# Kernel optimization log

Measured on AMD Instinct MI355X. Metric: run time of the kernel, lower is better.

Reference implementation:

```python
import jax, jax.numpy as jnp
import numpy as np

D = 256; HD = 16; G = 16; L = 2; HOP = 2; HK = 4
N = 16384; E = 49152; B = 256
VA = 128; VB = 8
SQRT2PI = float(np.sqrt(2.0 * 3.14159))  # module uses pi=3.14159


def group_norm(x, g=G, eps=1e-5):
    # torch GroupNorm(affine=False) on [N, D, 1]: normalize over each group of D//g channels
    n, d = x.shape
    xg = x.reshape(n, g, d // g)
    m = xg.mean(-1, keepdims=True)
    v = ((xg - m) ** 2).mean(-1, keepdims=True)
    return ((xg - m) * jax.lax.rsqrt(v + eps)).reshape(n, d)


def glin(x, w):
    # grouped 1x1 conv (no bias): x [n, g*din], w [g, dout, din] -> [n, g*dout]
    g, dout, din = w.shape
    return jnp.einsum('ngd,god->ngo', x.reshape(-1, g, din), w).reshape(-1, g * dout)


def multi_embed(idx, tables):
    # OGB-style encoder: sum of per-feature embeddings. idx [M,F], tables [F,V,D]
    out = tables[0][idx[:, 0]]
    for f in range(1, tables.shape[0]):
        out = out + tables[f][idx[:, f]]
    return out


def glb(x, pre_w, pre_b, gate_w, val_w, post_w, post_b):
    # GatedLinearBlock (dropout is identity in eval)
    xx = group_norm(x @ pre_w.T + pre_b)
    xx = jax.nn.relu(glin(xx, gate_w)) * glin(xx, val_w)
    return xx @ post_w.T + post_b


def glb2(xg, xv, gate_w, val_w, post_w, post_b):
    # GatedLinearBlock2: separate gate/value inputs, GroupNorm first
    gg = jax.nn.relu(glin(group_norm(xg), gate_w))
    vv = glin(group_norm(xv), val_w)
    return (gg * vv) @ post_w.T + post_b


def forward_impl(x_feat, edge_index, edge_attr, batch, batch_size,
                 edge_distance, atom_emb, bond2d_emb, gauss_means, gauss_stds,
                 attn_w, attn_b, scale_both,
                 conv_bond_emb, conv_pre_w, conv_gate_w, conv_val_w, conv_post_w, conv_post_b, conv_scale,
                 virt_pre_w, virt_pre_b, virt_gate_w, virt_val_w, virt_post_w, virt_post_b, virt_scale,
                 att_pre_w, att_pre_b, att_q_w, att_k_w, att_v_w, att_post_w, att_post_b, att_scale,
                 main_pre_w, main_pre_b, main_gate_w, main_val_w, main_post_w, main_post_b):
    src, dst = edge_index[0], edge_index[1]
    n = x_feat.shape[0]
    deg = jnp.clip(jax.ops.segment_sum(jnp.ones_like(dst), dst, num_segments=n) - 1, 0, 3)
    # --- edge features, mode='both': fuse 2D bond embedding with 3D gaussian features ---
    h2d = multi_embed(edge_attr, bond2d_emb)                      # [E, D]
    std = jnp.abs(gauss_stds) + 0.01
    diff = (edge_distance[:, None] - gauss_means[None, :]) / std
    h3d = jnp.exp(-0.5 * diff * diff) / (SQRT2PI * std)          # [E, D]
    w = jax.nn.sigmoid(jnp.concatenate([h2d, h3d], axis=-1) @ attn_w + attn_b[0])[:, None]
    h_e = w * h2d + (1.0 - w) * h3d
    h_in = jnp.exp(scale_both)[deg] * jax.ops.segment_sum(h_e, dst, num_segments=n)
    h_in = multi_embed(x_feat, atom_emb) + h_in                   # [N, D]
    h_virt = jnp.zeros((batch_size, D), h_in.dtype)
    h_att = jnp.zeros((batch_size, 2 * D // HD, HD, HD), h_in.dtype)
    for l in range(L):
        # --- ConvMessage: hop*kernel gated message-passing sublayers ---
        x_raw, x_out = h_in, jnp.zeros_like(h_in)
        for k in range(HK):
            if k > 0 and k % HOP == 0:
                x_raw, x_out = h_in + x_out, jnp.zeros_like(h_in)
            bond = multi_embed(edge_attr, conv_bond_emb[l, k])
            xp = x_raw @ conv_pre_w[l, k].T
            msg = glb2(xp[dst] + bond, xp[src] + bond,
                       conv_gate_w[l, k], conv_val_w[l, k], conv_post_w[l, k], conv_post_b[l, k])
            x_raw = jax.ops.segment_sum(msg, dst, num_segments=n)
            x_out = x_out + jnp.exp(conv_scale[l, k])[deg] * x_raw
        h_out = h_in + x_out
        # --- VirtMessage: graph-level virtual node with residual state ---
        h_virt = jax.ops.segment_sum(h_in, batch, num_segments=batch_size) + h_virt
        h_out = h_out + (jnp.exp(virt_scale[l]) * glb(h_virt, virt_pre_w[l], virt_pre_b[l],
                          virt_gate_w[l], virt_val_w[l], virt_post_w[l], virt_post_b[l]))[batch]
        # --- AttMessage: linear attention with per-graph scatter normalization ---
        xv0 = group_norm(h_in @ att_pre_w[l].T + att_pre_b[l])
        xq = jnp.exp(glin(xv0, att_q_w[l]) / np.sqrt(HD)).reshape(n, -1, HD)   # [N,32,16]
        xk = jnp.exp(glin(xv0, att_k_w[l]) / np.sqrt(HD)).reshape(n, -1, HD)
        xv = glin(xv0, att_v_w[l]).reshape(n, -1, HD)
        xkv = jnp.einsum('bnh,bnv->bnhv', xk, xv)                               # [N,32,16,16]
        h_att = jax.ops.segment_sum(xkv, batch, num_segments=batch_size) + h_att
        xk_sum = jax.ops.segment_sum(xk, batch, num_segments=batch_size)[batch]
        xq = xq / jnp.einsum('bnh,bnh->bn', xq, xk_sum)[:, :, None]
        att_out = jnp.einsum('bnh,bnhv->bnv', xq, h_att[batch]).reshape(n, 2 * D)
        h_out = h_out + jnp.exp(att_scale[l]) * (att_out @ att_post_w[l].T + att_post_b[l])
        # --- main gated block ---
        h_in = glb(h_out, main_pre_w[l], main_pre_b[l],
                   main_gate_w[l], main_val_w[l], main_post_w[l], main_post_b[l])
    return h_in


def setup_inputs() -> dict:
    key = jax.random.key(0)
    ks = iter(jax.random.split(key, 80))
    def rn(shape, s=0.05):
        return jax.random.normal(next(ks), shape, dtype=jnp.float32) * s
    inp = {}
    inp['x_feat'] = jax.random.randint(next(ks), (N, 9), 0, VA)
    inp['edge_index'] = jax.random.randint(next(ks), (2, E), 0, N)
    inp['edge_attr'] = jax.random.randint(next(ks), (E, 3), 0, VB)
    inp['batch'] = jnp.sort(jax.random.randint(next(ks), (N,), 0, B))
    inp['batch_size'] = B
    inp['edge_distance'] = jax.random.uniform(next(ks), (E,), dtype=jnp.float32) * 4.0
    inp['atom_emb'] = rn((9, VA, D))
    inp['bond2d_emb'] = rn((3, VB, D))
    inp['gauss_means'] = jax.random.uniform(next(ks), (D,), minval=2.0, maxval=3.0)
    inp['gauss_stds'] = jax.random.uniform(next(ks), (D,), minval=1.0, maxval=1.5)
    inp['attn_w'] = rn((2 * D,))
    inp['attn_b'] = rn((1,))
    inp['scale_both'] = jnp.full((4, D), np.log(0.1), jnp.float32)
    inp['conv_bond_emb'] = rn((L, HK, 3, VB, D))
    inp['conv_pre_w'] = rn((L, HK, D, D))
    inp['conv_gate_w'] = rn((L, HK, G, HD, HD))
    inp['conv_val_w'] = rn((L, HK, G, HD, HD))
    inp['conv_post_w'] = rn((L, HK, D, D))
    inp['conv_post_b'] = rn((L, HK, D))
    inp['conv_scale'] = jnp.full((L, HK, 4, D), np.log(0.1), jnp.float32)
    inp['virt_pre_w'] = rn((L, D, D)); inp['virt_pre_b'] = rn((L, D))
    inp['virt_gate_w'] = rn((L, G, 2 * HD, HD)); inp['virt_val_w'] = rn((L, G, 2 * HD, HD))
    inp['virt_post_w'] = rn((L, D, 2 * D)); inp['virt_post_b'] = rn((L, D))
    inp['virt_scale'] = jnp.full((L, D), np.log(0.01), jnp.float32)
    inp['att_pre_w'] = rn((L, D, D)); inp['att_pre_b'] = rn((L, D))
    inp['att_q_w'] = rn((L, G, 2 * HD, HD)); inp['att_k_w'] = rn((L, G, 2 * HD, HD)); inp['att_v_w'] = rn((L, G, 2 * HD, HD))
    inp['att_post_w'] = rn((L, D, 2 * D)); inp['att_post_b'] = rn((L, D))
    inp['att_scale'] = jnp.full((L, D), np.log(0.01), jnp.float32)
    inp['main_pre_w'] = rn((L, D, D)); inp['main_pre_b'] = rn((L, D))
    inp['main_gate_w'] = rn((L, G, 3 * HD, HD)); inp['main_val_w'] = rn((L, G, 3 * HD, HD))
    inp['main_post_w'] = rn((L, D, 3 * D)); inp['main_post_b'] = rn((L, D))
    return inp


def reference(x_feat, edge_index, edge_attr, batch, batch_size, edge_distance,
              atom_emb, bond2d_emb, gauss_means, gauss_stds, attn_w, attn_b, scale_both,
              conv_bond_emb, conv_pre_w, conv_gate_w, conv_val_w, conv_post_w, conv_post_b, conv_scale,
              virt_pre_w, virt_pre_b, virt_gate_w, virt_val_w, virt_post_w, virt_post_b, virt_scale,
              att_pre_w, att_pre_b, att_q_w, att_k_w, att_v_w, att_post_w, att_post_b, att_scale,
              main_pre_w, main_pre_b, main_gate_w, main_val_w, main_post_w, main_post_b):
    return forward_impl(x_feat, edge_index, edge_attr, batch, batch_size,
                        edge_distance, atom_emb, bond2d_emb, gauss_means, gauss_stds,
                        attn_w, attn_b, scale_both,
                        conv_bond_emb, conv_pre_w, conv_gate_w, conv_val_w, conv_post_w, conv_post_b, conv_scale,
                        virt_pre_w, virt_pre_b, virt_gate_w, virt_val_w, virt_post_w, virt_post_b, virt_scale,
                        att_pre_w, att_pre_b, att_q_w, att_k_w, att_v_w, att_post_w, att_post_b, att_scale,
                        main_pre_w, main_pre_b, main_gate_w, main_val_w, main_post_w, main_post_b)
```

## Files before the change

### kernel.cpp

```cpp
#include <hip/hip_runtime.h>
#include <cstdint>
#include <cstddef>
#include <type_traits>

#define NN 16384
#define EE 49152
#define BB 256

typedef _Float16 f16;
typedef _Float16 half8 __attribute__((ext_vector_type(8)));
typedef _Float16 half4v __attribute__((ext_vector_type(4)));
typedef _Float16 half2v __attribute__((ext_vector_type(2)));
typedef float floatx4 __attribute__((ext_vector_type(4)));

#if defined(__has_builtin)
#if __has_builtin(__builtin_amdgcn_fdot2)
#define HAVE_FDOT2 1
#endif
#endif

static constexpr size_t ND = (size_t)NN * 256;


__global__ __launch_bounds__(256) void count_deg_kernel(const int* __restrict__ dst, int* __restrict__ cnt, int e) {
  int i = blockIdx.x * 256 + threadIdx.x;
  if (i < e) atomicAdd(&cnt[dst[i]], 1);
}
__global__ __launch_bounds__(256) void clip_deg_kernel(const int* __restrict__ cnt, int* __restrict__ deg, int n) {
  int i = blockIdx.x * 256 + threadIdx.x;
  if (i < n) { int v = cnt[i] - 1; deg[i] = v < 0 ? 0 : (v > 3 ? 3 : v); }
}
__global__ __launch_bounds__(256) void goff_kernel(const int* __restrict__ batch, int* __restrict__ goff, int n, int b) {
  int i = blockIdx.x * 256 + threadIdx.x;
  if (i > n) return;
  int cur = (i < n) ? batch[i] : b;
  int prev = (i == 0) ? -1 : batch[i - 1];
  for (int x = prev + 1; x <= cur; x++) goff[x] = i;
}
__global__ __launch_bounds__(256) void scan_off_kernel(const int* __restrict__ cnt, int* __restrict__ off) {
  __shared__ int part[256];
  int tid = threadIdx.x;
  int base = tid * 64;
  int s = 0;
  for (int i = 0; i < 64; i++) s += cnt[base + i];
  part[tid] = s;
  __syncthreads();
  for (int o = 1; o < 256; o <<= 1) {
    int t = (tid >= o) ? part[tid - o] : 0;
    __syncthreads();
    part[tid] += t;
    __syncthreads();
  }
  int run = (tid == 0) ? 0 : part[tid - 1];
  for (int i = 0; i < 64; i++) {
    off[base + i] = run;
    run += cnt[base + i];
  }
  if (tid == 255) off[NN] = run;
}
__global__ __launch_bounds__(256) void copy_i_kernel(const int* __restrict__ a, int* __restrict__ b, int n) {
  int i = blockIdx.x * 256 + threadIdx.x;
  if (i < n) b[i] = a[i];
}
__global__ __launch_bounds__(256) void fill_elist_kernel(const int* __restrict__ dst,
    int* __restrict__ cursor, int* __restrict__ elist, int e) {
  int i = blockIdx.x * 256 + threadIdx.x;
  if (i < e) {
    int p = atomicAdd(&cursor[dst[i]], 1);
    elist[p] = i;
  }
}
__global__ __launch_bounds__(256) void gather_edges_kernel(const int* __restrict__ elist,
    const int* __restrict__ eattr, const int* __restrict__ src, const int* __restrict__ dst,
    const float* __restrict__ edist, int* __restrict__ ea_s, int* __restrict__ src_s,
    int* __restrict__ dst_s, float* __restrict__ ed_s) {
  int j = blockIdx.x * 256 + threadIdx.x;
  if (j >= EE) return;
  int e = elist[j];
  ea_s[j * 3 + 0] = eattr[e * 3 + 0];
  ea_s[j * 3 + 1] = eattr[e * 3 + 1];
  ea_s[j * 3 + 2] = eattr[e * 3 + 2];
  src_s[j] = src[e];
  dst_s[j] = dst[e];
  ed_s[j] = edist[e];
}
__global__ __launch_bounds__(256) void add3h_kernel(f16* __restrict__ dstH,
    const float* __restrict__ a, const float* __restrict__ b, int n4) {
  int i = blockIdx.x * 256 + threadIdx.x;
  if (i >= n4) return;
  float4 x = reinterpret_cast<const float4*>(a)[i];
  float4 y = reinterpret_cast<const float4*>(b)[i];
  half4v h;
  h[0] = (f16)(x.x + y.x); h[1] = (f16)(x.y + y.y);
  h[2] = (f16)(x.z + y.z); h[3] = (f16)(x.w + y.w);
  reinterpret_cast<half4v*>(dstH)[i] = h;
}
__global__ __launch_bounds__(256) void cvt6_kernel(
    const float* __restrict__ s0, const float* __restrict__ s1, const float* __restrict__ s2,
    const float* __restrict__ s3, const float* __restrict__ s4, const float* __restrict__ s5,
    f16* __restrict__ d0, f16* __restrict__ d1, f16* __restrict__ d2,
    f16* __restrict__ d3, f16* __restrict__ d4, f16* __restrict__ d5) {
  int i = blockIdx.x * 256 + threadIdx.x;
  const float* s;
  f16* d;
  int local;
  if (i < 131072)       { s = s0; d = d0; local = i; }
  else if (i < 262144)  { s = s1; d = d1; local = i - 131072; }
  else if (i < 294912)  { s = s2; d = d2; local = i - 262144; }
  else if (i < 360448)  { s = s3; d = d3; local = i - 294912; }
  else if (i < 393216)  { s = s4; d = d4; local = i - 360448; }
  else                  { s = s5; d = d5; local = i - 393216; }
  float4 v = reinterpret_cast<const float4*>(s)[local];
  half4v o;
  o[0] = (f16)v.x; o[1] = (f16)v.y; o[2] = (f16)v.z; o[3] = (f16)v.w;
  reinterpret_cast<half4v*>(d)[local] = o;
}

template <typename OUT>
__global__ __launch_bounds__(256) void seg_reduce_kernel(const f16* __restrict__ msg,
    const int* __restrict__ off, OUT* __restrict__ out) {
  int idx = blockIdx.x * 256 + threadIdx.x;
  int n = idx >> 6, c0 = (idx & 63) * 4;
  int j0 = off[n], j1 = off[n + 1];
  float a0 = 0.f, a1 = 0.f, a2 = 0.f, a3 = 0.f;
  int j = j0;
  for (; j + 1 < j1; j += 2) {
    half4v m0 = *reinterpret_cast<const half4v*>(&msg[(size_t)j * 256 + c0]);
    half4v m1 = *reinterpret_cast<const half4v*>(&msg[(size_t)(j + 1) * 256 + c0]);
    a0 += (float)m0[0] + (float)m1[0];
    a1 += (float)m0[1] + (float)m1[1];
    a2 += (float)m0[2] + (float)m1[2];
    a3 += (float)m0[3] + (float)m1[3];
  }
  if (j < j1) {
    half4v m0 = *reinterpret_cast<const half4v*>(&msg[(size_t)j * 256 + c0]);
    a0 += (float)m0[0]; a1 += (float)m0[1]; a2 += (float)m0[2]; a3 += (float)m0[3];
  }
  if constexpr (std::is_same<OUT, float>::value) {
    float4 o = {a0, a1, a2, a3};
    *reinterpret_cast<float4*>(&out[(size_t)n * 256 + c0]) = o;
  } else {
    half4v o;
    o[0] = (f16)a0; o[1] = (f16)a1; o[2] = (f16)a2; o[3] = (f16)a3;
    *reinterpret_cast<half4v*>(&out[(size_t)n * 256 + c0]) = o;
  }
}


__global__ __launch_bounds__(256) void edge_feat_kernel(
    const int* __restrict__ ea_s, const float* __restrict__ ed_s,
    const float* __restrict__ bond2d, const float* __restrict__ gmeans,
    const float* __restrict__ gstds, const float* __restrict__ attn_w,
    const float* __restrict__ attn_b, f16* __restrict__ msg) {
  int lane = threadIdx.x & 63;
  int j = blockIdx.x * 4 + (threadIdx.x >> 6);
  if (j >= EE) return;
  int a0 = ea_s[j * 3 + 0], a1 = ea_s[j * 3 + 1], a2 = ea_s[j * 3 + 2];
  float dist = ed_s[j];
  const float SQ2PI = sqrtf(2.0f * 3.14159f);
  int c0 = lane * 4;
  float4 b0 = *reinterpret_cast<const float4*>(&bond2d[a0 * 256 + c0]);
  float4 b1 = *reinterpret_cast<const float4*>(&bond2d[2048 + a1 * 256 + c0]);
  float4 b2 = *reinterpret_cast<const float4*>(&bond2d[4096 + a2 * 256 + c0]);
  float4 gm = *reinterpret_cast<const float4*>(&gmeans[c0]);
  float4 gs = *reinterpret_cast<const float4*>(&gstds[c0]);
  float4 w2 = *reinterpret_cast<const float4*>(&attn_w[c0]);
  float4 w3 = *reinterpret_cast<const float4*>(&attn_w[256 + c0]);
  float h2[4], h3[4];
  float part = 0.f;
#pragma unroll
  for (int i = 0; i < 4; i++) {
    h2[i] = (&b0.x)[i] + (&b1.x)[i] + (&b2.x)[i];
    float sd = fabsf((&gs.x)[i]) + 0.01f;
    float df = (dist - (&gm.x)[i]) / sd;
    h3[i] = expf(-0.5f * df * df) / (SQ2PI * sd);
    part += (&w2.x)[i] * h2[i] + (&w3.x)[i] * h3[i];
  }
#pragma unroll
  for (int off = 32; off > 0; off >>= 1) part += __shfl_xor(part, off);
  float wg = 1.f / (1.f + expf(-(part + attn_b[0])));
  half4v o;
#pragma unroll
  for (int i = 0; i < 4; i++) o[i] = (f16)(wg * h2[i] + (1.f - wg) * h3[i]);
  *reinterpret_cast<half4v*>(&msg[(size_t)j * 256 + c0]) = o;
}

__global__ __launch_bounds__(256) void atom_finish_kernel(
    const int* __restrict__ xf, const float* __restrict__ emb,
    const float* __restrict__ scale_both, const int* __restrict__ deg,
    const float* __restrict__ tmp, float* __restrict__ h_in, f16* __restrict__ h_inH) {
  int idx = blockIdx.x * 256 + threadIdx.x;
  int n = idx >> 6, c = (idx & 63) * 4;
  float a0 = 0.f, a1 = 0.f, a2 = 0.f, a3 = 0.f;
#pragma unroll
  for (int f = 0; f < 9; f++) {
    int v = xf[n * 9 + f];
    float4 e = *reinterpret_cast<const float4*>(&emb[((size_t)(f * 128 + v)) * 256 + c]);
    a0 += e.x; a1 += e.y; a2 += e.z; a3 += e.w;
  }
  int dg = deg[n];
  float4 s = *reinterpret_cast<const float4*>(&scale_both[dg * 256 + c]);
  float4 t = *reinterpret_cast<const float4*>(&tmp[(size_t)n * 256 + c]);
  float4 r;
  r.x = a0 + expf(s.x) * t.x; r.y = a1 + expf(s.y) * t.y;
  r.z = a2 + expf(s.z) * t.z; r.w = a3 + expf(s.w) * t.w;
  *reinterpret_cast<float4*>(&h_in[(size_t)n * 256 + c]) = r;
  half4v h;
  h[0] = (f16)r.x; h[1] = (f16)r.y; h[2] = (f16)r.z; h[3] = (f16)r.w;
  *reinterpret_cast<half4v*>(&h_inH[(size_t)n * 256 + c]) = h;
}

template <int MODE>
__global__ __launch_bounds__(256) void hgemm_kernel(
    const f16* __restrict__ A, const f16* __restrict__ W,
    const float* __restrict__ bias, const float* __restrict__ scale,
    const int* __restrict__ cnt, const int* __restrict__ deg,
    float* __restrict__ C, float* __restrict__ Cadd, f16* __restrict__ Cf,
    const float* __restrict__ vs2, const float* __restrict__ vout2,
    const int* __restrict__ batch2, int K) {
  __shared__ f16 Ah[64 * 40];
  __shared__ f16 Wh[64 * 40];
  const int tid = threadIdx.x;
  const int row0 = blockIdx.x * 64, col0 = blockIdx.y * 64;
  const int lane = tid & 63;
  const int wave = tid >> 6;
  const int wr = (wave >> 1) * 32, wc = (wave & 1) * 32;
  const floatx4 fz = {0.f, 0.f, 0.f, 0.f};
  floatx4 acc[2][2];
#pragma unroll
  for (int m = 0; m < 2; m++)
#pragma unroll
    for (int n = 0; n < 2; n++) acc[m][n] = fz;
  const int rS = tid >> 2, pS = tid & 3;
  const int kb = (lane >> 4) * 8;
  const int fr = lane & 15;
  uint4 a0 = *reinterpret_cast<const uint4*>(&A[(size_t)(row0 + rS) * K + pS * 8]);
  uint4 w0 = *reinterpret_cast<const uint4*>(&W[(size_t)(col0 + rS) * K + pS * 8]);
  for (int k0 = 0;;) {
    *reinterpret_cast<uint4*>(&Ah[rS * 40 + pS * 8]) = a0;
    *reinterpret_cast<uint4*>(&Wh[rS * 40 + pS * 8]) = w0;
    __syncthreads();
    int kn = k0 + 32;
    if (kn < K) {
      a0 = *reinterpret_cast<const uint4*>(&A[(size_t)(row0 + rS) * K + kn + pS * 8]);
      w0 = *reinterpret_cast<const uint4*>(&W[(size_t)(col0 + rS) * K + kn + pS * 8]);
    }
    half8 af[2], wf[2];
#pragma unroll
    for (int m = 0; m < 2; m++)
      af[m] = *reinterpret_cast<const half8*>(&Ah[(wr + m * 16 + fr) * 40 + kb]);
#pragma unroll
    for (int n = 0; n < 2; n++)
      wf[n] = *reinterpret_cast<const half8*>(&Wh[(wc + n * 16 + fr) * 40 + kb]);
#pragma unroll
    for (int m = 0; m < 2; m++)
#pragma unroll
      for (int n = 0; n < 2; n++)
        acc[m][n] = __builtin_amdgcn_mfma_f32_16x16x32_f16(af[m], wf[n], acc[m][n], 0, 0, 0);
    if (kn >= K) break;
    __syncthreads();
    k0 = kn;
  }
  const int rl4 = (lane >> 4) * 4, cl = lane & 15;
#pragma unroll
  for (int m = 0; m < 2; m++) {
#pragma unroll
    for (int i = 0; i < 4; i++) {
      int row = row0 + wr + m * 16 + rl4 + i;
      float cb = (MODE == 4 || MODE == 5) ? (float)cnt[row] : 1.f;
      int dg = (MODE == 4 || MODE == 5) ? deg[row] : 0;
      int brow = (MODE == 7) ? batch2[row] : 0;
#pragma unroll
      for (int n = 0; n < 2; n++) {
        int col = col0 + wc + n * 16 + cl;
        float v = acc[m][n][i];
        size_t oi = (size_t)row * 256 + col;
        if (MODE == 4 || MODE == 5) {
          v += cb * bias[col];
          float sc = expf(scale[dg * 256 + col]);
          if (MODE == 4) Cadd[oi] += sc * v;
          else Cadd[oi] = sc * v;
          if (Cf) Cf[oi] = (f16)v;
        } else if (MODE == 7) {
          v += bias[col];
          float nv = C[oi] + Cadd[oi] + expf(vs2[col]) * vout2[(size_t)brow * 256 + col]
                   + expf(scale[col]) * v;
          Cf[oi] = (f16)nv;
        } else if (MODE == 6) {
          v += bias[col];
          float s1 = v, s2 = v * v;
#pragma unroll
          for (int o_ = 1; o_ < 16; o_ <<= 1) {
            s1 += __shfl_xor(s1, o_);
            s2 += __shfl_xor(s2, o_);
          }
          float mean = s1 * (1.f / 16.f);
          float var = s2 * (1.f / 16.f) - mean * mean;
          float gnv = (v - mean) * rsqrtf(var + 1e-5f);
          if (C) C[oi] = gnv;
          if (Cf) Cf[oi] = (f16)gnv;
        } else {
          if (bias) v += bias[col];
          if (C) C[oi] = v;
          if (Cf) Cf[oi] = (f16)v;
        }
      }
    }
  }
}

__global__ __launch_bounds__(256) void conv_edge_kernel(
    const f16* __restrict__ xp, const int* __restrict__ ea_s,
    const int* __restrict__ src_s, const int* __restrict__ dst_s,
    const float* __restrict__ bond_emb, const float* __restrict__ gate_w,
    const float* __restrict__ val_w, f16* __restrict__ msg) {
  constexpr int RS = 264;
  __shared__ f16 sg[16 * RS];
  __shared__ f16 sv[16 * RS];
  int tid = threadIdx.x;
  for (int i = tid; i < 4096; i += 256) {
    int g = i >> 8, rem = i & 255;
    sg[g * RS + rem] = (f16)gate_w[i];
    sv[g * RS + rem] = (f16)val_w[i];
  }
  __syncthreads();
  int idx = blockIdx.x * 256 + tid;
  int j = idx >> 4, g = idx & 15;
  int a0 = ea_s[j * 3 + 0], a1 = ea_s[j * 3 + 1], a2 = ea_s[j * 3 + 2];
  int d = dst_s[j], s = src_s[j];
  half8 xd0 = *reinterpret_cast<const half8*>(&xp[(size_t)d * 256 + g * 16]);
  half8 xd1 = *reinterpret_cast<const half8*>(&xp[(size_t)d * 256 + g * 16 + 8]);
  half8 xs0 = *reinterpret_cast<const half8*>(&xp[(size_t)s * 256 + g * 16]);
  half8 xs1 = *reinterpret_cast<const half8*>(&xp[(size_t)s * 256 + g * 16 + 8]);
  const float4* b0p = reinterpret_cast<const float4*>(&bond_emb[a0 * 256 + g * 16]);
  const float4* b1p = reinterpret_cast<const float4*>(&bond_emb[2048 + a1 * 256 + g * 16]);
  const float4* b2p = reinterpret_cast<const float4*>(&bond_emb[4096 + a2 * 256 + g * 16]);
  float xg[16], xv[16];
  float mg = 0.f, mv = 0.f;
#pragma unroll
  for (int q = 0; q < 4; q++) {
    float4 b0 = b0p[q], b1 = b1p[q], b2 = b2p[q];
#pragma unroll
    for (int t = 0; t < 4; t++) {
      int i = q * 4 + t;
      float bo = (&b0.x)[t] + (&b1.x)[t] + (&b2.x)[t];
      float xd = (i < 8) ? (float)xd0[i & 7] : (float)xd1[i & 7];
      float xs = (i < 8) ? (float)xs0[i & 7] : (float)xs1[i & 7];
      xg[i] = xd + bo;
      xv[i] = xs + bo;
      mg += xg[i];
      mv += xv[i];
    }
  }
  mg *= (1.f / 16.f);
  mv *= (1.f / 16.f);
  float vg = 0.f, vv = 0.f;
#pragma unroll
  for (int i = 0; i < 16; i++) {
    float dg_ = xg[i] - mg, dv_ = xv[i] - mv;
    vg += dg_ * dg_;
    vv += dv_ * dv_;
  }
  float rg = rsqrtf(vg * (1.f / 16.f) + 1e-5f);
  float rv = rsqrtf(vv * (1.f / 16.f) + 1e-5f);
#ifdef HAVE_FDOT2
  half2v xgh[8], xvh[8];
#pragma unroll
  for (int q = 0; q < 8; q++) {
    xgh[q][0] = (f16)((xg[2 * q] - mg) * rg);
    xgh[q][1] = (f16)((xg[2 * q + 1] - mg) * rg);
    xvh[q][0] = (f16)((xv[2 * q] - mv) * rv);
    xvh[q][1] = (f16)((xv[2 * q + 1] - mv) * rv);
  }
#else
#pragma unroll
  for (int i = 0; i < 16; i++) {
    xg[i] = (xg[i] - mg) * rg;
    xv[i] = (xv[i] - mv) * rv;
  }
#endif
  const f16* gRow = &sg[g * RS];
  const f16* vRow = &sv[g * RS];
  f16 res[16];
#pragma unroll
  for (int o = 0; o < 16; o++) {
    half8 gA = *reinterpret_cast<const half8*>(&gRow[o * 16]);
    half8 gB = *reinterpret_cast<const half8*>(&gRow[o * 16 + 8]);
    half8 vA = *reinterpret_cast<const half8*>(&vRow[o * 16]);
    half8 vB = *reinterpret_cast<const half8*>(&vRow[o * 16 + 8]);
    float ag = 0.f, av = 0.f;
#ifdef HAVE_FDOT2
#pragma unroll
    for (int q = 0; q < 4; q++) {
      half2v ga = {gA[2 * q], gA[2 * q + 1]};
      half2v gb = {gB[2 * q], gB[2 * q + 1]};
      half2v va = {vA[2 * q], vA[2 * q + 1]};
      half2v vb = {vB[2 * q], vB[2 * q + 1]};
      ag = __builtin_amdgcn_fdot2(xgh[q], ga, ag, false);
      ag = __builtin_amdgcn_fdot2(xgh[q + 4], gb, ag, false);
      av = __builtin_amdgcn_fdot2(xvh[q], va, av, false);
      av = __builtin_amdgcn_fdot2(xvh[q + 4], vb, av, false);
    }
#else
#pragma unroll
    for (int i = 0; i < 8; i++) {
      ag += xg[i] * (float)gA[i] + xg[i + 8] * (float)gB[i];
      av += xv[i] * (float)vA[i] + xv[i + 8] * (float)vB[i];
    }
#endif
    res[o] = (f16)(fmaxf(ag, 0.f) * av);
  }
  uint4* op = reinterpret_cast<uint4*>(&msg[(size_t)j * 256 + g * 16]);
  op[0] = reinterpret_cast<const uint4*>(res)[0];
  op[1] = reinterpret_cast<const uint4*>(res)[1];
}

template <int DOUT>
__global__ __launch_bounds__(256) void glb_mid_h_kernel(
    const f16* __restrict__ X, const float* __restrict__ gate_w,
    const float* __restrict__ val_w, f16* __restrict__ out) {
  constexpr int RS = DOUT * 16 + 8;
  __shared__ f16 sg[16 * RS];
  __shared__ f16 sv[16 * RS];
  int tid = threadIdx.x;
  for (int i = tid; i < 16 * DOUT * 16; i += 256) {
    int g = i / (DOUT * 16), rem = i % (DOUT * 16);
    sg[g * RS + rem] = (f16)gate_w[i];
    sv[g * RS + rem] = (f16)val_w[i];
  }
  __syncthreads();
  int idx = blockIdx.x * 256 + tid;
  int n = idx >> 4, g = idx & 15;
  half8 x0 = *reinterpret_cast<const half8*>(&X[(size_t)n * 256 + g * 16]);
  half8 x1 = *reinterpret_cast<const half8*>(&X[(size_t)n * 256 + g * 16 + 8]);
#ifdef HAVE_FDOT2
  half2v xh[8];
#pragma unroll
  for (int q = 0; q < 4; q++) {
    xh[q][0] = x0[2 * q]; xh[q][1] = x0[2 * q + 1];
    xh[q + 4][0] = x1[2 * q]; xh[q + 4][1] = x1[2 * q + 1];
  }
#else
  float x[16];
#pragma unroll
  for (int i = 0; i < 8; i++) { x[i] = (float)x0[i]; x[i + 8] = (float)x1[i]; }
#endif
  const f16* gRow = &sg[g * RS];
  const f16* vRow = &sv[g * RS];
  f16 res[DOUT];
#pragma unroll
  for (int o = 0; o < DOUT; o++) {
    half8 gA = *reinterpret_cast<const half8*>(&gRow[o * 16]);
    half8 gB = *reinterpret_cast<const half8*>(&gRow[o * 16 + 8]);
    half8 vA = *reinterpret_cast<const half8*>(&vRow[o * 16]);
    half8 vB = *reinterpret_cast<const half8*>(&vRow[o * 16 + 8]);
    float ag = 0.f, av = 0.f;
#ifdef HAVE_FDOT2
#pragma unroll
    for (int q = 0; q < 4; q++) {
      half2v gq = {gA[2 * q], gA[2 * q + 1]};
      half2v g2 = {gB[2 * q], gB[2 * q + 1]};
      half2v vq = {vA[2 * q], vA[2 * q + 1]};
      half2v v2 = {vB[2 * q], vB[2 * q + 1]};
      ag = __builtin_amdgcn_fdot2(xh[q], gq, ag, false);
      ag = __builtin_amdgcn_fdot2(xh[q + 4], g2, ag, false);
      av = __builtin_amdgcn_fdot2(xh[q], vq, av, false);
      av = __builtin_amdgcn_fdot2(xh[q + 4], v2, av, false);
    }
#else
#pragma unroll
    for (int i = 0; i < 8; i++) {
      ag += x[i] * (float)gA[i] + x[i + 8] * (float)gB[i];
      av += x[i] * (float)vA[i] + x[i + 8] * (float)vB[i];
    }
#endif
    res[o] = (f16)(fmaxf(ag, 0.f) * av);
  }
  f16* op = &out[(size_t)n * (16 * DOUT) + g * DOUT];
#pragma unroll
  for (int q = 0; q < DOUT / 8; q++)
    *reinterpret_cast<half8*>(&op[q * 8]) = *reinterpret_cast<const half8*>(&res[q * 8]);
}

__global__ __launch_bounds__(256) void virt_fused_kernel(
    const float* __restrict__ h_in, const int* __restrict__ goff,
    const float* __restrict__ preW, const float* __restrict__ preb,
    const float* __restrict__ gateW, const float* __restrict__ valW,
    const float* __restrict__ postW, const float* __restrict__ postb,
    float* __restrict__ h_virt, float* __restrict__ vout) {
  __shared__ float sred[4][256];
  __shared__ float sx[256];
  __shared__ float xx[256];
  __shared__ float vv[512];
  int tid = threadIdx.x, b = blockIdx.x;
  int n0 = goff[b], n1 = goff[b + 1];
  int sub = tid >> 6, cg = tid & 63;
  float a0 = 0.f, a1 = 0.f, a2 = 0.f, a3 = 0.f;
  for (int n = n0 + sub; n < n1; n += 4) {
    float4 x = *reinterpret_cast<const float4*>(&h_in[(size_t)n * 256 + cg * 4]);
    a0 += x.x; a1 += x.y; a2 += x.z; a3 += x.w;
  }
  sred[sub][cg * 4 + 0] = a0;
  sred[sub][cg * 4 + 1] = a1;
  sred[sub][cg * 4 + 2] = a2;
  sred[sub][cg * 4 + 3] = a3;
  __syncthreads();
  float acc = h_virt[(size_t)b * 256 + tid] + sred[0][tid] + sred[1][tid] + sred[2][tid] + sred[3][tid];
  h_virt[(size_t)b * 256 + tid] = acc;
  sx[tid] = acc;
  __syncthreads();
  float dot = preb[tid];
  const float4* wrow = reinterpret_cast<const float4*>(&preW[(size_t)tid * 256]);
  const float4* sx4 = reinterpret_cast<const float4*>(sx);
#pragma unroll 8
  for (int q = 0; q < 64; q++) {
    float4 w = wrow[q];
    float4 s = sx4[q];
    dot += w.x * s.x + w.y * s.y + w.z * s.z + w.w * s.w;
  }
  float s1 = dot, s2 = dot * dot;
#pragma unroll
  for (int o_ = 1; o_ < 16; o_ <<= 1) {
    s1 += __shfl_xor(s1, o_);
    s2 += __shfl_xor(s2, o_);
  }
  float mean = s1 * (1.f / 16.f);
  float var = s2 * (1.f / 16.f) - mean * mean;
  xx[tid] = (dot - mean) * rsqrtf(var + 1e-5f);
  __syncthreads();
#pragma unroll
  for (int rep = 0; rep < 2; rep++) {
    int o = tid + rep * 256;
    int g = o >> 5, o2 = o & 31;
    const float4* gw = reinterpret_cast<const float4*>(&gateW[(size_t)(g * 32 + o2) * 16]);
    const float4* vw = reinterpret_cast<const float4*>(&valW[(size_t)(g * 32 + o2) * 16]);
    const float4* xg4 = reinterpret_cast<const float4*>(&xx[g * 16]);
    float ag = 0.f, av = 0.f;
#pragma unroll
    for (int q = 0; q < 4; q++) {
      float4 wg = gw[q], wv = vw[q], xq = xg4[q];
      ag += wg.x * xq.x + wg.y * xq.y + wg.z * xq.z + wg.w * xq.w;
      av += wv.x * xq.x + wv.y * xq.y + wv.z * xq.z + wv.w * xq.w;
    }
    vv[o] = fmaxf(ag, 0.f) * av;
  }
  __syncthreads();
  float outv = postb[tid];
  const float4* prow = reinterpret_cast<const float4*>(&postW[(size_t)tid * 512]);
  const float4* vv4 = reinterpret_cast<const float4*>(vv);
#pragma unroll 8
  for (int q = 0; q < 128; q++) {
    float4 w = prow[q], s = vv4[q];
    outv += w.x * s.x + w.y * s.y + w.z * s.z + w.w * s.w;
  }
  vout[(size_t)b * 256 + tid] = outv;
}

template <bool FIRST>
__global__ __launch_bounds__(256) void att_graph_kernel(
    const float* __restrict__ xv0, const float* __restrict__ k_w,
    const float* __restrict__ v_w, const int* __restrict__ goff,
    float* __restrict__ h_att, float* __restrict__ xk_sum) {
  __shared__ float kx[8][256];
  __shared__ float vx[8][256];
  __shared__ float rows[8][256];
  const int tid = threadIdx.x;
  const int b = blockIdx.x >> 1, half = blockIdx.x & 1;
  const int p = half * 256 + tid;
  const int g = p >> 5;
  const int headLocal = tid >> 4;
  const int head = p >> 4, h = p & 15;
  float wk[16], wv[16];
#pragma unroll
  for (int i = 0; i < 4; i++) {
    float4 k0 = *reinterpret_cast<const float4*>(&k_w[p * 16 + i * 4]);
    float4 v0 = *reinterpret_cast<const float4*>(&v_w[p * 16 + i * 4]);
    wk[i * 4 + 0] = k0.x; wk[i * 4 + 1] = k0.y; wk[i * 4 + 2] = k0.z; wk[i * 4 + 3] = k0.w;
    wv[i * 4 + 0] = v0.x; wv[i * 4 + 1] = v0.y; wv[i * 4 + 2] = v0.z; wv[i * 4 + 3] = v0.w;
  }
  float hacc[16];
  if (FIRST) {
#pragma unroll
    for (int j = 0; j < 16; j++) hacc[j] = 0.f;
  } else {
    const float* hg = &h_att[(size_t)b * 8192];
#pragma unroll
    for (int j = 0; j < 16; j++) hacc[j] = hg[h * 512 + head * 16 + j];
  }
  float ks = 0.f;
  const int n0 = goff[b], n1 = goff[b + 1];
  float r[8];
#pragma unroll
  for (int nn = 0; nn < 8; nn++) {
    int n = n0 + nn;
    r[nn] = (n < n1) ? xv0[(size_t)n * 256 + tid] : 0.f;
  }
  for (int nbase = n0; nbase < n1; nbase += 8) {
#pragma unroll
    for (int nn = 0; nn < 8; nn++) rows[nn][tid] = r[nn];
    __syncthreads();
#pragma unroll
    for (int nn = 0; nn < 8; nn++) {
      int n = nbase + 8 + nn;
      r[nn] = (n < n1) ? xv0[(size_t)n * 256 + tid] : 0.f;
    }
#pragma unroll
    for (int nn = 0; nn < 8; nn++) {
      const float4* rp = reinterpret_cast<const float4*>(&rows[nn][g * 16]);
      float aK = 0.f, aV = 0.f;
#pragma unroll
      for (int q = 0; q < 4; q++) {
        float4 x0 = rp[q];
#pragma unroll
        for (int t = 0; t < 4; t++) {
          float e0 = (&x0.x)[t];
          aK += e0 * wk[q * 4 + t];
          aV += e0 * wv[q * 4 + t];
        }
      }
      bool valid = (nbase + nn) < n1;
      float ek = valid ? expf(aK * 0.25f) : 0.f;
      kx[nn][tid] = ek;
      vx[nn][tid] = aV;
      ks += ek;
    }
    __syncthreads();
#pragma unroll
    for (int nn = 0; nn < 8; nn++) {
      float kk = kx[nn][tid];
      const float4* vp = reinterpret_cast<const float4*>(&vx[nn][headLocal * 16]);
#pragma unroll
      for (int q = 0; q < 4; q++) {
        float4 vq = vp[q];
        hacc[q * 4 + 0] += kk * vq.x;
        hacc[q * 4 + 1] += kk * vq.y;
        hacc[q * 4 + 2] += kk * vq.z;
        hacc[q * 4 + 3] += kk * vq.w;
      }
    }
    __syncthreads();
  }
  float* hgo = &h_att[(size_t)b * 8192];
#pragma unroll
  for (int j = 0; j < 16; j++) hgo[h * 512 + head * 16 + j] = hacc[j];
  xk_sum[(size_t)b * 512 + p] = ks;
}

__global__ __launch_bounds__(256) void att_out_kernel(
    const float* __restrict__ xv0, const float* __restrict__ q_w,
    const float* __restrict__ xk_sum, const float* __restrict__ h_att,
    const int* __restrict__ goff, f16* __restrict__ out) {
  __shared__ float sqw[16 * 260];
  __shared__ float hat[16 * 644];
  int tid = threadIdx.x, b = blockIdx.x;
  for (int i = tid; i < 8192; i += 256) {
    int g = i >> 9, rem = i & 511;
    sqw[g * 260 + rem] = q_w[i];
  }
  for (int i = tid; i < 8192; i += 256) {
    int h = i >> 9, rem = i & 511;
    int head = rem >> 4, v = rem & 15;
    hat[h * 644 + head * 20 + v] = h_att[(size_t)b * 8192 + i];
  }
  __syncthreads();
  int n0 = goff[b], n1 = goff[b + 1];
  int nl = tid >> 5, head = tid & 31;
  int g = head >> 1, j = head & 1;
  const float* ks = &xk_sum[(size_t)b * 512 + head * 16];
  for (int nbase = n0; nbase < n1; nbase += 8) {
    int n = nbase + nl;
    if (n >= n1) continue;
    float x[16];
    const float4* xp4 = reinterpret_cast<const float4*>(&xv0[(size_t)n * 256 + g * 16]);
#pragma unroll
    for (int q = 0; q < 4; q++) {
      float4 xq = xp4[q];
#pragma unroll
      for (int t = 0; t < 4; t++) x[q * 4 + t] = (&xq.x)[t];
    }
    float qv[16];
    float denom = 0.f;
#pragma unroll
    for (int h = 0; h < 16; h++) {
      const float4* wp = reinterpret_cast<const float4*>(&sqw[g * 260 + (j * 16 + h) * 16]);
      float a = 0.f;
#pragma unroll
      for (int q = 0; q < 4; q++) {
        float4 wq = wp[q];
#pragma unroll
        for (int t = 0; t < 4; t++) a += x[q * 4 + t] * (&wq.x)[t];
      }
      float e = expf(a * 0.25f);
      qv[h] = e;
      denom += e * ks[h];
    }
    float inv = 1.f / denom;
    float acc[16] = {0.f, 0.f, 0.f, 0.f, 0.f, 0.f, 0.f, 0.f,
                     0.f, 0.f, 0.f, 0.f, 0.f, 0.f, 0.f, 0.f};
#pragma unroll
    for (int h = 0; h < 16; h++) {
      float qh = qv[h];
      const float4* hp = reinterpret_cast<const float4*>(&hat[h * 644 + head * 20]);
#pragma unroll
      for (int q = 0; q < 4; q++) {
        float4 vq = hp[q];
        acc[q * 4 + 0] += qh * vq.x;
        acc[q * 4 + 1] += qh * vq.y;
        acc[q * 4 + 2] += qh * vq.z;
        acc[q * 4 + 3] += qh * vq.w;
      }
    }
    f16 res[16];
#pragma unroll
    for (int v = 0; v < 16; v++) res[v] = (f16)(acc[v] * inv);
    uint4* op = reinterpret_cast<uint4*>(&out[(size_t)n * 512 + head * 16]);
    op[0] = reinterpret_cast<const uint4*>(res)[0];
    op[1] = reinterpret_cast<const uint4*>(res)[1];
  }
}


extern "C" void kernel_launch(void* const* d_in, const int* in_sizes, int n_in,
                              void* d_out, int out_size, void* d_ws, size_t ws_size,
                              hipStream_t stream) {
  const int* x_feat = (const int*)d_in[0];
  const int* eidx = (const int*)d_in[1];
  const int* eattr = (const int*)d_in[2];
  const int* batch = (const int*)d_in[3];
  const float* edist = (const float*)d_in[5];
  const float* atom_emb = (const float*)d_in[6];
  const float* bond2d = (const float*)d_in[7];
  const float* gmeans = (const float*)d_in[8];
  const float* gstds = (const float*)d_in[9];
  const float* attn_w = (const float*)d_in[10];
  const float* attn_b = (const float*)d_in[11];
  const float* scale_both = (const float*)d_in[12];
  const float* conv_bond_emb = (const float*)d_in[13];
  const float* conv_pre_w = (const float*)d_in[14];
  const float* conv_gate_w = (const float*)d_in[15];
  const float* conv_val_w = (const float*)d_in[16];
  const float* conv_post_w = (const float*)d_in[17];
  const float* conv_post_b = (const float*)d_in[18];
  const float* conv_scale = (const float*)d_in[19];
  const float* virt_pre_w = (const float*)d_in[20];
  const float* virt_pre_b = (const float*)d_in[21];
  const float* virt_gate_w = (const float*)d_in[22];
  const float* virt_val_w = (const float*)d_in[23];
  const float* virt_post_w = (const float*)d_in[24];
  const float* virt_post_b = (const float*)d_in[25];
  const float* virt_scale = (const float*)d_in[26];
  const float* att_pre_w = (const float*)d_in[27];
  const float* att_pre_b = (const float*)d_in[28];
  const float* att_q_w = (const float*)d_in[29];
  const float* att_k_w = (const float*)d_in[30];
  const float* att_v_w = (const float*)d_in[31];
  const float* att_post_w = (const float*)d_in[32];
  const float* att_post_b = (const float*)d_in[33];
  const float* att_scale = (const float*)d_in[34];
  const float* main_pre_w = (const float*)d_in[35];
  const float* main_pre_b = (const float*)d_in[36];
  const float* main_gate_w = (const float*)d_in[37];
  const float* main_val_w = (const float*)d_in[38];
  const float* main_post_w = (const float*)d_in[39];
  const float* main_post_b = (const float*)d_in[40];

  const int* src = eidx;
  const int* dst = eidx + EE;

  float* ws = (float*)d_ws;
  float* h_in = ws;
  float* x_out = ws + ND;
  float* nodeA = ws + 2 * ND;
  f16* h_inH = (f16*)(ws + 3 * ND);
  f16* xrawH = (f16*)(ws + 3 * ND + ND / 2);
  f16* hTmp = (f16*)(ws + 4 * ND);
  f16* gnH = (f16*)(ws + 4 * ND + ND / 2);
  f16* msgH = (f16*)(ws + 5 * ND);
  float* sm = ws + 7 * ND;
  f16* hW = (f16*)sm;
  float* h_virt = sm + 1179648;
  float* h_att = h_virt + 65536;
  float* xk_sum = h_att + 2097152;
  float* vout = xk_sum + 131072;
  int* cnt = (int*)(vout + 65536);
  int* deg = cnt + NN;
  int* goff = deg + NN;
  int* off = goff + BB + 1;
  int* cursor = off + NN + 1;
  int* elist = cursor + NN;
  int* ea_s = elist + EE;
  int* src_s = ea_s + 3 * EE;
  int* dst_s = src_s + EE;
  float* ed_s = (float*)(dst_s + EE);

  f16* wCpre = hW;
  f16* wCpost = hW + 524288;
  f16* wApre = hW + 1048576;
  f16* wApost = hW + 1179648;
  f16* wMpre = hW + 1441792;
  f16* wMpost = hW + 1572864;

  cvt6_kernel<<<491520 / 256, 256, 0, stream>>>(
      conv_pre_w, conv_post_w, att_pre_w, att_post_w, main_pre_w, main_post_w,
      wCpre, wCpost, wApre, wApost, wMpre, wMpost);

  (void)hipMemsetAsync(cnt, 0, NN * sizeof(int), stream);
  count_deg_kernel<<<EE / 256, 256, 0, stream>>>(dst, cnt, EE);
  clip_deg_kernel<<<NN / 256, 256, 0, stream>>>(cnt, deg, NN);
  goff_kernel<<<(NN + 256) / 256, 256, 0, stream>>>(batch, goff, NN, BB);
  scan_off_kernel<<<1, 256, 0, stream>>>(cnt, off);
  copy_i_kernel<<<NN / 256, 256, 0, stream>>>(off, cursor, NN);
  fill_elist_kernel<<<EE / 256, 256, 0, stream>>>(dst, cursor, elist, EE);
  gather_edges_kernel<<<EE / 256, 256, 0, stream>>>(elist, eattr, src, dst, edist,
                                                    ea_s, src_s, dst_s, ed_s);

  edge_feat_kernel<<<EE / 4, 256, 0, stream>>>(ea_s, ed_s, bond2d, gmeans, gstds,
                                               attn_w, attn_b, msgH);
  seg_reduce_kernel<float><<<NN / 4, 256, 0, stream>>>(msgH, off, x_out);
  atom_finish_kernel<<<NN * 64 / 256, 256, 0, stream>>>(x_feat, atom_emb, scale_both, deg,
                                                        x_out, h_in, h_inH);
  (void)hipMemsetAsync(h_virt, 0, 65536 * 4, stream);

  const dim3 gN(NN / 64, 4);
  const int n4 = (int)(ND / 4);

  for (int l = 0; l < 2; l++) {
    const f16* curH = h_inH;
    for (int k = 0; k < 4; k++) {
      if (k == 2) {
        add3h_kernel<<<n4 / 256, 256, 0, stream>>>(xrawH, h_in, x_out, n4);
        curH = xrawH;
      }
      size_t lk = (size_t)(l * 4 + k);
      hgemm_kernel<0><<<gN, 256, 0, stream>>>(curH, wCpre + lk * 65536, nullptr, nullptr,
                                              nullptr, nullptr, nullptr, nullptr, hTmp,
                                              nullptr, nullptr, nullptr, 256);
      conv_edge_kernel<<<EE * 16 / 256, 256, 0, stream>>>(
          hTmp, ea_s, src_s, dst_s, conv_bond_emb + lk * 6144,
          conv_gate_w + lk * 4096, conv_val_w + lk * 4096, msgH);
      seg_reduce_kernel<f16><<<NN / 4, 256, 0, stream>>>(msgH, off, gnH);
      if (k == 0 || k == 2)
        hgemm_kernel<5><<<gN, 256, 0, stream>>>(gnH, wCpost + lk * 65536,
                                                conv_post_b + lk * 256, conv_scale + lk * 1024,
                                                cnt, deg, nullptr, x_out, xrawH,
                                                nullptr, nullptr, nullptr, 256);
      else
        hgemm_kernel<4><<<gN, 256, 0, stream>>>(gnH, wCpost + lk * 65536,
                                                conv_post_b + lk * 256, conv_scale + lk * 1024,
                                                cnt, deg, nullptr, x_out, xrawH,
                                                nullptr, nullptr, nullptr, 256);
      curH = xrawH;
    }

    virt_fused_kernel<<<BB, 256, 0, stream>>>(
        h_in, goff, virt_pre_w + (size_t)l * 65536, virt_pre_b + (size_t)l * 256,
        virt_gate_w + (size_t)l * 8192, virt_val_w + (size_t)l * 8192,
        virt_post_w + (size_t)l * 131072, virt_post_b + (size_t)l * 256, h_virt, vout);

    hgemm_kernel<6><<<gN, 256, 0, stream>>>(h_inH, wApre + (size_t)l * 65536,
                                            att_pre_b + (size_t)l * 256, nullptr, nullptr,
                                            nullptr, nodeA, nullptr, nullptr,
                                            nullptr, nullptr, nullptr, 256);
    if (l == 0)
      att_graph_kernel<true><<<BB * 2, 256, 0, stream>>>(
          nodeA, att_k_w + (size_t)l * 8192, att_v_w + (size_t)l * 8192, goff, h_att, xk_sum);
    else
      att_graph_kernel<false><<<BB * 2, 256, 0, stream>>>(
          nodeA, att_k_w + (size_t)l * 8192, att_v_w + (size_t)l * 8192, goff, h_att, xk_sum);
    att_out_kernel<<<BB, 256, 0, stream>>>(
        nodeA, att_q_w + (size_t)l * 8192, xk_sum, h_att, goff, msgH);
    hgemm_kernel<7><<<gN, 256, 0, stream>>>(msgH, wApost + (size_t)l * 131072,
                                            att_post_b + (size_t)l * 256,
                                            att_scale + (size_t)l * 256, nullptr, nullptr,
                                            h_in, x_out, hTmp,
                                            virt_scale + (size_t)l * 256, vout, batch, 512);

    hgemm_kernel<6><<<gN, 256, 0, stream>>>(hTmp, wMpre + (size_t)l * 65536,
                                            main_pre_b + (size_t)l * 256, nullptr, nullptr,
                                            nullptr, nullptr, nullptr, gnH,
                                            nullptr, nullptr, nullptr, 256);
    glb_mid_h_kernel<48><<<NN * 16 / 256, 256, 0, stream>>>(
        gnH, main_gate_w + (size_t)l * 12288, main_val_w + (size_t)l * 12288, msgH);
    float* hdst = (l == 1) ? (float*)d_out : h_in;
    f16* hdstH = (l == 1) ? nullptr : h_inH;
    hgemm_kernel<0><<<gN, 256, 0, stream>>>(msgH, wMpost + (size_t)l * 196608,
                                            main_post_b + (size_t)l * 256, nullptr, nullptr,
                                            nullptr, hdst, nullptr, hdstH,
                                            nullptr, nullptr, nullptr, 768);
  }
}
```

Before: 910.4 us.

## Fuse segment-sum of edge messages into conv post GEMM A-tile load

Removes the separate seg_reduce launch and its f16 intermediate write/read in each conv step. The post-projection GEMM now builds its full 64x256 A tile in shared memory by summing CSR-ordered edge messages per row. The trade-off is that each column block (gN has several y-blocks) repeats the same gather-reduce, so message reads are duplicated. Shared memory per block also grows, which may lower occupancy.

Result: slower. 960.8 us (+5.5%).

```diff
diff --git a/kernel.cpp b/kernel.cpp
--- a/kernel.cpp
+++ b/kernel.cpp
@@ -116,34 +116,18 @@
   reinterpret_cast<half4v*>(d)[local] = o;
 }
 
-template <typename OUT>
-__global__ __launch_bounds__(256) void seg_reduce_kernel(const f16* __restrict__ msg,
-    const int* __restrict__ off, OUT* __restrict__ out) {
+__global__ __launch_bounds__(256) void seg_reduce_f_kernel(const f16* __restrict__ msg,
+    const int* __restrict__ off, float* __restrict__ out) {
   int idx = blockIdx.x * 256 + threadIdx.x;
   int n = idx >> 6, c0 = (idx & 63) * 4;
   int j0 = off[n], j1 = off[n + 1];
   float a0 = 0.f, a1 = 0.f, a2 = 0.f, a3 = 0.f;
-  int j = j0;
-  for (; j + 1 < j1; j += 2) {
-    half4v m0 = *reinterpret_cast<const half4v*>(&msg[(size_t)j * 256 + c0]);
-    half4v m1 = *reinterpret_cast<const half4v*>(&msg[(size_t)(j + 1) * 256 + c0]);
-    a0 += (float)m0[0] + (float)m1[0];
-    a1 += (float)m0[1] + (float)m1[1];
-    a2 += (float)m0[2] + (float)m1[2];
-    a3 += (float)m0[3] + (float)m1[3];
-  }
-  if (j < j1) {
+  for (int j = j0; j < j1; j++) {
     half4v m0 = *reinterpret_cast<const half4v*>(&msg[(size_t)j * 256 + c0]);
     a0 += (float)m0[0]; a1 += (float)m0[1]; a2 += (float)m0[2]; a3 += (float)m0[3];
   }
-  if constexpr (std::is_same<OUT, float>::value) {
-    float4 o = {a0, a1, a2, a3};
-    *reinterpret_cast<float4*>(&out[(size_t)n * 256 + c0]) = o;
-  } else {
-    half4v o;
-    o[0] = (f16)a0; o[1] = (f16)a1; o[2] = (f16)a2; o[3] = (f16)a3;
-    *reinterpret_cast<half4v*>(&out[(size_t)n * 256 + c0]) = o;
-  }
+  float4 o = {a0, a1, a2, a3};
+  *reinterpret_cast<float4*>(&out[(size_t)n * 256 + c0]) = o;
 }
 
 
@@ -210,15 +194,16 @@
   *reinterpret_cast<half4v*>(&h_inH[(size_t)n * 256 + c]) = h;
 }
 
-template <int MODE>
+template <int MODE, int SEGA>
 __global__ __launch_bounds__(256) void hgemm_kernel(
     const f16* __restrict__ A, const f16* __restrict__ W,
     const float* __restrict__ bias, const float* __restrict__ scale,
-    const int* __restrict__ cnt, const int* __restrict__ deg,
+    const int* __restrict__ cnt, const int* __restrict__ deg, const int* __restrict__ offA,
     float* __restrict__ C, float* __restrict__ Cadd, f16* __restrict__ Cf,
     const float* __restrict__ vs2, const float* __restrict__ vout2,
     const int* __restrict__ batch2, int K) {
-  __shared__ f16 Ah[64 * 40];
+  constexpr int ARS = SEGA ? 264 : 40;
+  __shared__ f16 Ah[64 * ARS];
   __shared__ f16 Wh[64 * 40];
   const int tid = threadIdx.x;
   const int row0 = blockIdx.x * 64, col0 = blockIdx.y * 64;
@@ -234,21 +219,40 @@
   const int rS = tid >> 2, pS = tid & 3;
   const int kb = (lane >> 4) * 8;
   const int fr = lane & 15;
-  uint4 a0 = *reinterpret_cast<const uint4*>(&A[(size_t)(row0 + rS) * K + pS * 8]);
-  uint4 w0 = *reinterpret_cast<const uint4*>(&W[(size_t)(col0 + rS) * K + pS * 8]);
+  if (SEGA) {
+#pragma unroll
+    for (int cc = 0; cc < 8; cc++) {
+      int c = tid + cc * 256;
+      int r = c >> 5, p = c & 31;
+      int j0 = offA[row0 + r], j1 = offA[row0 + r + 1];
+      float s[8] = {0.f, 0.f, 0.f, 0.f, 0.f, 0.f, 0.f, 0.f};
+      for (int j = j0; j < j1; j++) {
+        half8 m = *reinterpret_cast<const half8*>(&A[(size_t)j * 256 + p * 8]);
+#pragma unroll
+        for (int t = 0; t < 8; t++) s[t] += (float)m[t];
+      }
+      half8 hv;
+#pragma unroll
+      for (int t = 0; t < 8; t++) hv[t] = (f16)s[t];
+      *reinterpret_cast<half8*>(&Ah[r * ARS + p * 8]) = hv;
+    }
+  }
+  uint4 a0, w0;
+  if (!SEGA) a0 = *reinterpret_cast<const uint4*>(&A[(size_t)(row0 + rS) * K + pS * 8]);
+  w0 = *reinterpret_cast<const uint4*>(&W[(size_t)(col0 + rS) * K + pS * 8]);
   for (int k0 = 0;;) {
-    *reinterpret_cast<uint4*>(&Ah[rS * 40 + pS * 8]) = a0;
+    if (!SEGA) *reinterpret_cast<uint4*>(&Ah[rS * 40 + pS * 8]) = a0;
     *reinterpret_cast<uint4*>(&Wh[rS * 40 + pS * 8]) = w0;
     __syncthreads();
     int kn = k0 + 32;
     if (kn < K) {
-      a0 = *reinterpret_cast<const uint4*>(&A[(size_t)(row0 + rS) * K + kn + pS * 8]);
+      if (!SEGA) a0 = *reinterpret_cast<const uint4*>(&A[(size_t)(row0 + rS) * K + kn + pS * 8]);
       w0 = *reinterpret_cast<const uint4*>(&W[(size_t)(col0 + rS) * K + kn + pS * 8]);
     }
     half8 af[2], wf[2];
 #pragma unroll
     for (int m = 0; m < 2; m++)
-      af[m] = *reinterpret_cast<const half8*>(&Ah[(wr + m * 16 + fr) * 40 + kb]);
+      af[m] = *reinterpret_cast<const half8*>(&Ah[(wr + m * 16 + fr) * ARS + (SEGA ? k0 : 0) + kb]);
 #pragma unroll
     for (int n = 0; n < 2; n++)
       wf[n] = *reinterpret_cast<const half8*>(&Wh[(wc + n * 16 + fr) * 40 + kb]);
@@ -816,7 +820,7 @@
 
   edge_feat_kernel<<<EE / 4, 256, 0, stream>>>(ea_s, ed_s, bond2d, gmeans, gstds,
                                                attn_w, attn_b, msgH);
-  seg_reduce_kernel<float><<<NN / 4, 256, 0, stream>>>(msgH, off, x_out);
+  seg_reduce_f_kernel<<<NN / 4, 256, 0, stream>>>(msgH, off, x_out);
   atom_finish_kernel<<<NN * 64 / 256, 256, 0, stream>>>(x_feat, atom_emb, scale_both, deg,
                                                         x_out, h_in, h_inH);
   (void)hipMemsetAsync(h_virt, 0, 65536 * 4, stream);
@@ -832,23 +836,24 @@
         curH = xrawH;
       }
       size_t lk = (size_t)(l * 4 + k);
-      hgemm_kernel<0><<<gN, 256, 0, stream>>>(curH, wCpre + lk * 65536, nullptr, nullptr,
-                                              nullptr, nullptr, nullptr, nullptr, hTmp,
-                                              nullptr, nullptr, nullptr, 256);
+      hgemm_kernel<0, 0><<<gN, 256, 0, stream>>>(curH, wCpre + lk * 65536, nullptr, nullptr,
+                                                 nullptr, nullptr, nullptr, nullptr, nullptr,
+                                                 hTmp, nullptr, nullptr, nullptr, 256);
       conv_edge_kernel<<<EE * 16 / 256, 256, 0, stream>>>(
           hTmp, ea_s, src_s, dst_s, conv_bond_emb + lk * 6144,
           conv_gate_w + lk * 4096, conv_val_w + lk * 4096, msgH);
-      seg_reduce_kernel<f16><<<NN / 4, 256, 0, stream>>>(msgH, off, gnH);
       if (k == 0 || k == 2)
-        hgemm_kernel<5><<<gN, 256, 0, stream>>>(gnH, wCpost + lk * 65536,
-                                                conv_post_b + lk * 256, conv_scale + lk * 1024,
-                                                cnt, deg, nullptr, x_out, xrawH,
-                                                nullptr, nullptr, nullptr, 256);
+        hgemm_kernel<5, 1><<<gN, 256, 0, stream>>>(msgH, wCpost + lk * 65536,
+                                                   conv_post_b + lk * 256,
+                                                   conv_scale + lk * 1024, cnt, deg, off,
+                                                   nullptr, x_out, xrawH,
+                                                   nullptr, nullptr, nullptr, 256);
       else
-        hgemm_kernel<4><<<gN, 256, 0, stream>>>(gnH, wCpost + lk * 65536,
-                                                conv_post_b + lk * 256, conv_scale + lk * 1024,
-                                                cnt, deg, nullptr, x_out, xrawH,
-                                                nullptr, nullptr, nullptr, 256);
+        hgemm_kernel<4, 1><<<gN, 256, 0, stream>>>(msgH, wCpost + lk * 65536,
+                                                   conv_post_b + lk * 256,
+                                                   conv_scale + lk * 1024, cnt, deg, off,
+                                                   nullptr, x_out, xrawH,
+                                                   nullptr, nullptr, nullptr, 256);
       curH = xrawH;
     }
 
@@ -857,10 +862,10 @@
         virt_gate_w + (size_t)l * 8192, virt_val_w + (size_t)l * 8192,
         virt_post_w + (size_t)l * 131072, virt_post_b + (size_t)l * 256, h_virt, vout);
 
-    hgemm_kernel<6><<<gN, 256, 0, stream>>>(h_inH, wApre + (size_t)l * 65536,
-                                            att_pre_b + (size_t)l * 256, nullptr, nullptr,
-                                            nullptr, nodeA, nullptr, nullptr,
-                                            nullptr, nullptr, nullptr, 256);
+    hgemm_kernel<6, 0><<<gN, 256, 0, stream>>>(h_inH, wApre + (size_t)l * 65536,
+                                               att_pre_b + (size_t)l * 256, nullptr, nullptr,
+                                               nullptr, nullptr, nodeA, nullptr, nullptr,
+                                               nullptr, nullptr, nullptr, 256);
     if (l == 0)
       att_graph_kernel<true><<<BB * 2, 256, 0, stream>>>(
           nodeA, att_k_w + (size_t)l * 8192, att_v_w + (size_t)l * 8192, goff, h_att, xk_sum);
@@ -869,23 +874,23 @@
           nodeA, att_k_w + (size_t)l * 8192, att_v_w + (size_t)l * 8192, goff, h_att, xk_sum);
     att_out_kernel<<<BB, 256, 0, stream>>>(
         nodeA, att_q_w + (size_t)l * 8192, xk_sum, h_att, goff, msgH);
-    hgemm_kernel<7><<<gN, 256, 0, stream>>>(msgH, wApost + (size_t)l * 131072,
-                                            att_post_b + (size_t)l * 256,
-                                            att_scale + (size_t)l * 256, nullptr, nullptr,
-                                            h_in, x_out, hTmp,
-                                            virt_scale + (size_t)l * 256, vout, batch, 512);
-
-    hgemm_kernel<6><<<gN, 256, 0, stream>>>(hTmp, wMpre + (size_t)l * 65536,
-                                            main_pre_b + (size_t)l * 256, nullptr, nullptr,
-                                            nullptr, nullptr, nullptr, gnH,
-                                            nullptr, nullptr, nullptr, 256);
+    hgemm_kernel<7, 0><<<gN, 256, 0, stream>>>(msgH, wApost + (size_t)l * 131072,
+                                               att_post_b + (size_t)l * 256,
+                                               att_scale + (size_t)l * 256, nullptr, nullptr,
+                                               nullptr, h_in, x_out, hTmp,
+                                               virt_scale + (size_t)l * 256, vout, batch, 512);
+
+    hgemm_kernel<6, 0><<<gN, 256, 0, stream>>>(hTmp, wMpre + (size_t)l * 65536,
+                                               main_pre_b + (size_t)l * 256, nullptr, nullptr,
+                                               nullptr, nullptr, nullptr, nullptr, gnH,
+                                               nullptr, nullptr, nullptr, 256);
     glb_mid_h_kernel<48><<<NN * 16 / 256, 256, 0, stream>>>(
         gnH, main_gate_w + (size_t)l * 12288, main_val_w + (size_t)l * 12288, msgH);
     float* hdst = (l == 1) ? (float*)d_out : h_in;
     f16* hdstH = (l == 1) ? nullptr : h_inH;
-    hgemm_kernel<0><<<gN, 256, 0, stream>>>(msgH, wMpost + (size_t)l * 196608,
-                                            main_post_b + (size_t)l * 256, nullptr, nullptr,
-                                            nullptr, hdst, nullptr, hdstH,
-                                            nullptr, nullptr, nullptr, 768);
-  }
-}
+    hgemm_kernel<0, 0><<<gN, 256, 0, stream>>>(msgH, wMpost + (size_t)l * 196608,
+                                               main_post_b + (size_t)l * 256, nullptr, nullptr,
+                                               nullptr, nullptr, hdst, nullptr, hdstH,
+                                               nullptr, nullptr, nullptr, 768);
+  }
+}
```
